# Kernel tuning notes

Hardware: AMD Instinct MI355X
Metric: run time of the kernel (lower is better)

Reference implementation:

```python
import jax, jax.numpy as jnp
import numpy as np

BETA = 8.0  # cfg.memory.beta (inverse temperature)
EPS = 1e-12  # matches F.normalize default eps


def _l2_normalize(x):
    return x / jnp.maximum(jnp.linalg.norm(x, axis=-1, keepdims=True), EPS)


def setup_inputs() -> dict:
    key = jax.random.key(0)
    k1, k2, k3 = jax.random.split(key, 3)
    embeddings = jax.random.normal(k1, (1024, 128), dtype=jnp.float32)   # queries [B, D]
    keys = jax.random.normal(k2, (100000, 128), dtype=jnp.float32)       # stored patterns [N, D]
    labels = jax.random.randint(k3, (100000,), 0, 1000)                  # class per stored pattern [N]
    return {"embeddings": embeddings, "keys": keys, "labels": labels, "n_classes": 1000}


def reference(embeddings, keys, labels, n_classes):
    # store(): keys normalized (normalize_keys=True); values = one_hot(labels)
    k = _l2_normalize(keys)
    # query(): normalize queries, cosine sims, softmax(beta*sims), weighted value sum
    q = _l2_normalize(embeddings)
    sims = q @ k.T                                   # [B, N]
    weights = jax.nn.softmax(BETA * sims, axis=-1)   # [B, N]
    # weights @ one_hot(labels, C) == segment-sum of weights by key label (same math,
    # avoids materializing the dense [N, C] one-hot value matrix)
    out = jax.ops.segment_sum(weights.T, labels, num_segments=n_classes).T  # [B, C]
    return out
```

## Files before the change

### kernel.cpp

```cpp
#include <hip/hip_runtime.h>
#include <math.h>

typedef _Float16 f16;
typedef _Float16 f16x8 __attribute__((ext_vector_type(8)));
typedef float    f32x16 __attribute__((ext_vector_type(16)));
typedef unsigned int uint;
typedef unsigned short u16;

#define B_Q     1024
#define DIM     128
#define N_KEYS  100000
#define NPAD    102400
#define NGP     (NPAD / 32)
#define GPC     8
#define NCHUNK  (NGP / GPC)
#define N_CLS   1000
#define QSCALE  11.541560327111707f
#define CSUM    10
#define NCB     (N_CLS / CSUM)
#define NH      128
#define QGRP    (B_Q / 32)

__global__ void k_hist(const int* __restrict__ labels, uint* __restrict__ hist128) {
    __shared__ uint lh[N_CLS];
    for (int i = threadIdx.x; i < N_CLS; i += blockDim.x) lh[i] = 0;
    __syncthreads();
    const int stride = gridDim.x * blockDim.x;
    for (int i = blockIdx.x * blockDim.x + threadIdx.x; i < N_KEYS; i += stride)
        atomicAdd(&lh[labels[i]], 1u);
    __syncthreads();
    for (int i = threadIdx.x; i < N_CLS; i += blockDim.x)
        hist128[blockIdx.x * N_CLS + i] = lh[i];
}

__global__ void k_scan(const uint* __restrict__ hist128, uint* __restrict__ cursor) {
    __shared__ uint s[1024];
    const int t = threadIdx.x;
    uint v = 0;
    if (t < N_CLS)
        for (int b = 0; b < NH; ++b) v += hist128[b * N_CLS + t];
    s[t] = v; __syncthreads();
    for (int o = 1; o < 1024; o <<= 1) {
        const uint x = (t >= o) ? s[t - o] : 0u;
        __syncthreads();
        s[t] += x;
        __syncthreads();
    }
    if (t < N_CLS) cursor[t] = s[t] - v;
}

__global__ void k_perm(const int* __restrict__ labels, uint* __restrict__ cursor,
                       int* __restrict__ src, u16* __restrict__ kcls) {
    const int n = blockIdx.x * blockDim.x + threadIdx.x;
    if (n >= NPAD) return;
    if (n < N_KEYS) {
        const int lab = labels[n];
        const int pos = (int)atomicAdd(&cursor[lab], 1u);
        src[pos]  = n;
        kcls[pos] = (u16)lab;
    } else {
        src[n]  = -1;
        kcls[n] = (u16)N_CLS;
    }
}

__global__ __launch_bounds__(256)
void k_gather(const float* __restrict__ qm, const float* __restrict__ km,
              const int* __restrict__ src, f16* __restrict__ kf2,
              f16* __restrict__ qf2) {
    __shared__ float ssq[8][32];
    __shared__ float scale[32];
    const int g = blockIdx.x;
    const int t = threadIdx.x;
    const int r = t & 31;
    const int p = t >> 5;
    const bool isq = g >= NGP;

    const float* srow;
    if (isq) srow = qm + (size_t)((g - NGP) * 32 + r) * DIM;
    else {
        const int sr = src[g * 32 + r];
        srow = (sr >= 0) ? km + (size_t)sr * DIM : nullptr;
    }

    float4 v[4];
    float ss = 0.0f;
    if (srow) {
        #pragma unroll
        for (int i = 0; i < 4; ++i) {
            v[i] = *(const float4*)(srow + p * 16 + i * 4);
            ss += v[i].x * v[i].x + v[i].y * v[i].y
                + v[i].z * v[i].z + v[i].w * v[i].w;
        }
    } else {
        #pragma unroll
        for (int i = 0; i < 4; ++i) v[i] = float4{0.f, 0.f, 0.f, 0.f};
    }
    ssq[p][r] = ss;
    __syncthreads();
    if (t < 32) {
        float s = 0.0f;
        #pragma unroll
        for (int i = 0; i < 8; ++i) s += ssq[i][t];
        scale[t] = (isq ? QSCALE : 1.0f) / fmaxf(sqrtf(s), 1e-12f);
    }
    __syncthreads();
    const float sc = scale[r];

    const float f[16] = {v[0].x, v[0].y, v[0].z, v[0].w,
                         v[1].x, v[1].y, v[1].z, v[1].w,
                         v[2].x, v[2].y, v[2].z, v[2].w,
                         v[3].x, v[3].y, v[3].z, v[3].w};
    f16x8 h0, h1;
    #pragma unroll
    for (int j = 0; j < 8; ++j) {
        h0[j] = (f16)(f[j]     * sc);
        h1[j] = (f16)(f[j + 8] * sc);
    }
    f16* dst = isq ? qf2 + (size_t)(g - NGP) * 4096
                   : kf2 + (size_t)g * 4096;
    *(f16x8*)(dst + p * 512 +       r * 8) = h0;
    *(f16x8*)(dst + p * 512 + 256 + r * 8) = h1;
}

__global__ void k_meta(const u16* __restrict__ kcls, int* __restrict__ meta,
                       float* __restrict__ out_t) {
    const int nt = gridDim.x * blockDim.x;
    const float4 z = {0.0f, 0.0f, 0.0f, 0.0f};
    for (int i = blockIdx.x * blockDim.x + threadIdx.x;
         i < N_CLS * B_Q / 4; i += nt)
        ((float4*)out_t)[i] = z;

    const int gid  = blockIdx.x * blockDim.x + threadIdx.x;
    const int g    = gid >> 6;
    const int lane = threadIdx.x & 63;
    if (g >= NGP) return;
    const int  cl = kcls[g * 32 + (lane & 31)];
    const int  ca = __shfl(cl, 0);
    const uint dm = (uint)(__ballot(cl != ca) & 0xffffffffull);
    const int  split = dm ? (__ffs(dm) - 1) : 32;
    const int  cb = (split < 32) ? __shfl(cl, split) : ca;
    if (lane == 0) meta[g] = ca | (cb << 11) | (split << 22);
}

#define FLUSH2(C) {                                                           \
        const float v0 = racc0 + __shfl_xor(racc0, 32);                       \
        const float v1 = racc1 + __shfl_xor(racc1, 32);                       \
        if (lhi == 0) {                                                       \
            atomicAdd(&out_t[(size_t)(C) * B_Q + q00 + l31], v0);             \
            atomicAdd(&out_t[(size_t)(C) * B_Q + q01 + l31], v1);             \
        }                                                                     \
    }

__global__ __launch_bounds__(256, 3)
void class_gemm6(const f16* __restrict__ kf2, const f16* __restrict__ qf2,
                 const int* __restrict__ meta, float* __restrict__ out_t) {
    const int tid  = threadIdx.x;
    const int w    = tid >> 6;
    const int lane = tid & 63;
    const int l31  = lane & 31;
    const int lhi  = lane >> 5;
    const int lhi4 = lhi << 2;

    const int b     = blockIdx.x;
    const int xcd   = b & 7;
    const int s     = b >> 3;
    const int chunk = xcd * (NCHUNK / 8) + (s >> 2);
    const int qquad = s & 3;
    const int g0    = chunk * GPC;

    f16x8 Q0[8], Q1[8];
    {
        const f16* qa = qf2 + (size_t)(qquad * 8 + w * 2) * 4096 + lane * 8;
        #pragma unroll
        for (int kk = 0; kk < 8; ++kk) {
            Q0[kk] = *(const f16x8*)(qa + kk * 512);
            Q1[kk] = *(const f16x8*)(qa + 4096 + kk * 512);
        }
    }
    const int q00 = qquad * 256 + w * 64;
    const int q01 = q00 + 32;

    const int mv = meta[g0 + (lane & (GPC - 1))];

    float racc0 = 0.0f, racc1 = 0.0f;
    int cur = -1;

    for (int i = 0; i < GPC; ++i) {
        const int m     = __shfl(mv, i);
        const int ca    = m & 0x7FF;
        const int cb    = (m >> 11) & 0x7FF;
        const int split = m >> 22;

        const f16* base = kf2 + (size_t)(g0 + i) * 4096 + lane * 8;
        f32x16 c0 = {}, c1 = {};
        #pragma unroll
        for (int kk = 0; kk < 8; ++kk) {
            const f16x8 Kf = *(const f16x8*)(base + kk * 512);
            c0 = __builtin_amdgcn_mfma_f32_32x32x16_f16(Kf, Q0[kk], c0, 0, 0, 0);
            c1 = __builtin_amdgcn_mfma_f32_32x32x16_f16(Kf, Q1[kk], c1, 0, 0, 0);
        }

        if (ca != cur) {
            if (cur >= 0) FLUSH2(cur);
            racc0 = 0.0f; racc1 = 0.0f;
            cur = ca;
        }
        if (split == 32) {
            float ga = 0.0f, gb = 0.0f, gc = 0.0f, gd = 0.0f;
            #pragma unroll
            for (int r = 0; r < 16; r += 2) {
                ga += __builtin_amdgcn_exp2f(c0[r]);
                gb += __builtin_amdgcn_exp2f(c0[r + 1]);
                gc += __builtin_amdgcn_exp2f(c1[r]);
                gd += __builtin_amdgcn_exp2f(c1[r + 1]);
            }
            racc0 += ga + gb;
            racc1 += gc + gd;
        } else {
            float ga = 0.0f, gb = 0.0f, gc = 0.0f, gd = 0.0f;
            float ha = 0.0f, hb = 0.0f, hc = 0.0f, hd = 0.0f;
            #pragma unroll
            for (int r = 0; r < 16; r += 2) {
                const int  kr0 = ((r & 3) + 8 * (r >> 2)) + lhi4;
                const int  kr1 = (((r + 1) & 3) + 8 * ((r + 1) >> 2)) + lhi4;
                const float e0  = __builtin_amdgcn_exp2f(c0[r]);
                const float e0b = __builtin_amdgcn_exp2f(c0[r + 1]);
                const float e1  = __builtin_amdgcn_exp2f(c1[r]);
                const float e1b = __builtin_amdgcn_exp2f(c1[r + 1]);
                const bool inA0 = kr0 < split;
                const bool inA1 = kr1 < split;
                ga += inA0 ? e0  : 0.0f;  ha += inA0 ? 0.0f : e0;
                gb += inA1 ? e0b : 0.0f;  hb += inA1 ? 0.0f : e0b;
                gc += inA0 ? e1  : 0.0f;  hc += inA0 ? 0.0f : e1;
                gd += inA1 ? e1b : 0.0f;  hd += inA1 ? 0.0f : e1b;
            }
            racc0 += ga + gb;
            racc1 += gc + gd;
            FLUSH2(cur);
            racc0 = ha + hb;
            racc1 = hc + hd;
            cur = cb;
        }
    }
    if (cur >= 0) FLUSH2(cur);
}

__global__ __launch_bounds__(1024)
void k_qsum(const float* __restrict__ out_t, float* __restrict__ partial) {
    const int cb = blockIdx.x;
    const int q  = threadIdx.x;
    const float* p = out_t + (size_t)cb * CSUM * B_Q + q;
    float s = 0.0f;
    #pragma unroll
    for (int i = 0; i < CSUM; ++i) s += p[(size_t)i * B_Q];
    partial[cb * B_Q + q] = s;
}

__global__ __launch_bounds__(256)
void k_norm_t(const float* __restrict__ out_t, const float* __restrict__ partial,
              float* __restrict__ out) {
    __shared__ float tile[64 * 65];
    __shared__ float invq[64];
    const int tid  = threadIdx.x;
    const int w    = tid >> 6;
    const int lane = tid & 63;
    const int q0   = blockIdx.x * 64;
    const int c0   = blockIdx.y * 64;

    if (tid < 64) {
        float s = 0.0f;
        for (int cb = 0; cb < NCB; ++cb) s += partial[cb * B_Q + q0 + tid];
        invq[tid] = 1.0f / s;
    }
    #pragma unroll
    for (int i = 0; i < 16; ++i) {
        const int cidx = c0 + w * 16 + i;
        const float v = (cidx < N_CLS) ? out_t[(size_t)cidx * B_Q + q0 + lane] : 0.0f;
        tile[lane * 65 + w * 16 + i] = v;
    }
    __syncthreads();
    #pragma unroll
    for (int j = 0; j < 16; ++j) {
        const int r    = w * 16 + j;
        const int cidx = c0 + lane;
        if (cidx < N_CLS)
            out[(size_t)(q0 + r) * N_CLS + cidx] = tile[r * 65 + lane] * invq[r];
    }
}

extern "C" void kernel_launch(void* const* d_in, const int* in_sizes, int n_in,
                              void* d_out, int out_size, void* d_ws, size_t ws_size,
                              hipStream_t stream) {
    const float* qm     = (const float*)d_in[0];
    const float* km     = (const float*)d_in[1];
    const int*   labels = (const int*)d_in[2];
    float* out = (float*)d_out;

    char* p = (char*)d_ws;
    f16*   kf2     = (f16*)p;   p += (size_t)NPAD * DIM * 2;
    f16*   qf2     = (f16*)p;   p += (size_t)B_Q * DIM * 2;
    float* out_t   = (float*)p; p += (size_t)N_CLS * B_Q * 4;
    float* partial = (float*)p; p += (size_t)NCB * B_Q * 4;
    uint*  cursor  = (uint*)p;  p += N_CLS * 4;
    u16*   kcls    = (u16*)p;   p += (size_t)NPAD * 2;
    int*   meta    = (int*)p;   p += (size_t)NGP * 4;
    int*   src     = (int*)p;   p += (size_t)NPAD * 4;
    uint*  hist128 = (uint*)out_t;

    hipLaunchKernelGGL(k_hist, dim3(NH), dim3(256), 0, stream, labels, hist128);
    hipLaunchKernelGGL(k_scan, dim3(1), dim3(1024), 0, stream, hist128, cursor);
    hipLaunchKernelGGL(k_perm, dim3(NPAD / 256), dim3(256), 0, stream,
                       labels, cursor, src, kcls);
    hipLaunchKernelGGL(k_gather, dim3(NGP + QGRP), dim3(256), 0, stream,
                       qm, km, src, kf2, qf2);
    hipLaunchKernelGGL(k_meta, dim3((NGP * 64 + 255) / 256), dim3(256), 0, stream,
                       kcls, meta, out_t);

    hipLaunchKernelGGL(class_gemm6, dim3(4 * NCHUNK), dim3(256), 0, stream,
                       kf2, qf2, meta, out_t);

    hipLaunchKernelGGL(k_qsum, dim3(NCB), dim3(1024), 0, stream, out_t, partial);
    hipLaunchKernelGGL(k_norm_t, dim3(B_Q / 64, (N_CLS + 63) / 64), dim3(256), 0, stream,
                       out_t, partial, out);
}
```

Baseline: 110.7 us.

## Split GEMM into single-wave blocks, double-buffer K loads, fuse query totals

Replaces the 4-wave GEMM blocks with one-wave blocks and register double-buffers the K fragments, so the next group's loads overlap the current MFMA and exp work. Per-query softmax denominators are now accumulated inside the GEMM through atomics into a qtot buffer, which removes the separate k_qsum pass. The extra zeroing range covers the padding sink row and qtot. This costs more blocks, more atomics and higher register pressure from holding two K buffers.

```diff
diff --git a/kernel.cpp b/kernel.cpp
--- a/kernel.cpp
+++ b/kernel.cpp
@@ -16,8 +16,6 @@
 #define NCHUNK  (NGP / GPC)
 #define N_CLS   1000
 #define QSCALE  11.541560327111707f
-#define CSUM    10
-#define NCB     (N_CLS / CSUM)
 #define NH      128
 #define QGRP    (B_Q / 32)
 
@@ -123,12 +121,12 @@
     *(f16x8*)(dst + p * 512 + 256 + r * 8) = h1;
 }
 
+#define ZFLOATS ((N_CLS + 2) * B_Q)
 __global__ void k_meta(const u16* __restrict__ kcls, int* __restrict__ meta,
                        float* __restrict__ out_t) {
     const int nt = gridDim.x * blockDim.x;
     const float4 z = {0.0f, 0.0f, 0.0f, 0.0f};
-    for (int i = blockIdx.x * blockDim.x + threadIdx.x;
-         i < N_CLS * B_Q / 4; i += nt)
+    for (int i = blockIdx.x * blockDim.x + threadIdx.x; i < ZFLOATS / 4; i += nt)
         ((float4*)out_t)[i] = z;
 
     const int gid  = blockIdx.x * blockDim.x + threadIdx.x;
@@ -146,119 +144,129 @@
 #define FLUSH2(C) {                                                           \
         const float v0 = racc0 + __shfl_xor(racc0, 32);                       \
         const float v1 = racc1 + __shfl_xor(racc1, 32);                       \
+        if ((C) != N_CLS) { tot0 += racc0; tot1 += racc1; }                   \
         if (lhi == 0) {                                                       \
             atomicAdd(&out_t[(size_t)(C) * B_Q + q00 + l31], v0);             \
             atomicAdd(&out_t[(size_t)(C) * B_Q + q01 + l31], v1);             \
         }                                                                     \
     }
 
-__global__ __launch_bounds__(256, 3)
-void class_gemm6(const f16* __restrict__ kf2, const f16* __restrict__ qf2,
-                 const int* __restrict__ meta, float* __restrict__ out_t) {
-    const int tid  = threadIdx.x;
-    const int w    = tid >> 6;
-    const int lane = tid & 63;
+#define LOADK(DST, I) {                                                       \
+        const f16* _kb = kf2 + (size_t)(g0 + (I)) * 4096 + lane * 8;          \
+        _Pragma("unroll")                                                     \
+        for (int kk = 0; kk < 8; ++kk) DST[kk] = *(const f16x8*)(_kb + kk * 512); \
+    }
+
+#define BODY(KB, I) {                                                         \
+        const int m     = __shfl(mv, (I));       \
+        const int ca    = m & 0x7FF;                                          \
+        const int cb    = (m >> 11) & 0x7FF;                                  \
+        const int split = m >> 22;                                            \
+        f32x16 c0 = {}, c1 = {};                                              \
+        _Pragma("unroll")                                                     \
+        for (int kk = 0; kk < 8; ++kk) {                                      \
+            c0 = __builtin_amdgcn_mfma_f32_32x32x16_f16(KB[kk], Q0[kk], c0, 0, 0, 0); \
+            c1 = __builtin_amdgcn_mfma_f32_32x32x16_f16(KB[kk], Q1[kk], c1, 0, 0, 0); \
+        }                                                                     \
+        if (ca != cur) {                                                      \
+            if (cur >= 0) FLUSH2(cur);                                        \
+            racc0 = 0.0f; racc1 = 0.0f;                                       \
+            cur = ca;                                                         \
+        }                                                                     \
+        if (split == 32) {                                                    \
+            float ga = 0.f, gb = 0.f, gc = 0.f, gd = 0.f;                     \
+            _Pragma("unroll")                                                 \
+            for (int r = 0; r < 16; r += 2) {                                 \
+                ga += __builtin_amdgcn_exp2f(c0[r]);                          \
+                gb += __builtin_amdgcn_exp2f(c0[r + 1]);                      \
+                gc += __builtin_amdgcn_exp2f(c1[r]);                          \
+                gd += __builtin_amdgcn_exp2f(c1[r + 1]);                      \
+            }                                                                 \
+            racc0 += ga + gb;                                                 \
+            racc1 += gc + gd;                                                 \
+        } else {                                                              \
+            float ga = 0.f, gb = 0.f, gc = 0.f, gd = 0.f;                     \
+            float ha = 0.f, hb = 0.f, hc = 0.f, hd = 0.f;                     \
+            _Pragma("unroll")                                                 \
+            for (int r = 0; r < 16; r += 2) {                                 \
+                const int  kr0 = ((r & 3) + 8 * (r >> 2)) + lhi4;             \
+                const int  kr1 = (((r + 1) & 3) + 8 * ((r + 1) >> 2)) + lhi4; \
+                const float e0  = __builtin_amdgcn_exp2f(c0[r]);              \
+                const float e0b = __builtin_amdgcn_exp2f(c0[r + 1]);          \
+                const float e1  = __builtin_amdgcn_exp2f(c1[r]);              \
+                const float e1b = __builtin_amdgcn_exp2f(c1[r + 1]);          \
+                const bool inA0 = kr0 < split;                                \
+                const bool inA1 = kr1 < split;                                \
+                ga += inA0 ? e0  : 0.0f;  ha += inA0 ? 0.0f : e0;             \
+                gb += inA1 ? e0b : 0.0f;  hb += inA1 ? 0.0f : e0b;            \
+                gc += inA0 ? e1  : 0.0f;  hc += inA0 ? 0.0f : e1;             \
+                gd += inA1 ? e1b : 0.0f;  hd += inA1 ? 0.0f : e1b;            \
+            }                                                                 \
+            racc0 += ga + gb;                                                 \
+            racc1 += gc + gd;                                                 \
+            FLUSH2(cur);                                                      \
+            racc0 = ha + hb;                                                  \
+            racc1 = hc + hd;                                                  \
+            cur = cb;                                                         \
+        }                                                                     \
+    }
+
+__global__ __launch_bounds__(64)
+void class_gemm7(const f16* __restrict__ kf2, const f16* __restrict__ qf2,
+                 const int* __restrict__ meta, float* __restrict__ out_t,
+                 float* __restrict__ qtot) {
+    const int lane = threadIdx.x & 63;
     const int l31  = lane & 31;
     const int lhi  = lane >> 5;
     const int lhi4 = lhi << 2;
 
     const int b     = blockIdx.x;
     const int xcd   = b & 7;
-    const int s     = b >> 3;
-    const int chunk = xcd * (NCHUNK / 8) + (s >> 2);
-    const int qquad = s & 3;
+    const int u     = b >> 3;
+    const int chunk = xcd * (NCHUNK / 8) + (u >> 4);
+    const int qquad = (u >> 2) & 3;
+    const int wsub  = u & 3;
     const int g0    = chunk * GPC;
 
     f16x8 Q0[8], Q1[8];
     {
-        const f16* qa = qf2 + (size_t)(qquad * 8 + w * 2) * 4096 + lane * 8;
+        const f16* qa = qf2 + (size_t)(qquad * 8 + wsub * 2) * 4096 + lane * 8;
         #pragma unroll
         for (int kk = 0; kk < 8; ++kk) {
             Q0[kk] = *(const f16x8*)(qa + kk * 512);
             Q1[kk] = *(const f16x8*)(qa + 4096 + kk * 512);
         }
     }
-    const int q00 = qquad * 256 + w * 64;
+    const int q00 = qquad * 256 + wsub * 64;
     const int q01 = q00 + 32;
 
     const int mv = meta[g0 + (lane & (GPC - 1))];
 
     float racc0 = 0.0f, racc1 = 0.0f;
+    float tot0  = 0.0f, tot1  = 0.0f;
     int cur = -1;
 
-    for (int i = 0; i < GPC; ++i) {
-        const int m     = __shfl(mv, i);
-        const int ca    = m & 0x7FF;
-        const int cb    = (m >> 11) & 0x7FF;
-        const int split = m >> 22;
-
-        const f16* base = kf2 + (size_t)(g0 + i) * 4096 + lane * 8;
-        f32x16 c0 = {}, c1 = {};
-        #pragma unroll
-        for (int kk = 0; kk < 8; ++kk) {
-            const f16x8 Kf = *(const f16x8*)(base + kk * 512);
-            c0 = __builtin_amdgcn_mfma_f32_32x32x16_f16(Kf, Q0[kk], c0, 0, 0, 0);
-            c1 = __builtin_amdgcn_mfma_f32_32x32x16_f16(Kf, Q1[kk], c1, 0, 0, 0);
+    f16x8 K0[8], K1[8];
+    LOADK(K0, 0);
+    #pragma unroll
+    for (int ii = 0; ii < GPC / 2; ++ii) {
+        { const int i = 2 * ii;     if (i + 1 < GPC) LOADK(K1, i + 1); BODY(K0, i); }
+        { const int i = 2 * ii + 1; if (i + 1 < GPC) LOADK(K0, i + 1); BODY(K1, i); }
+    }
+    if (cur >= 0) FLUSH2(cur);
+
+    {
+        const float t0 = tot0 + __shfl_xor(tot0, 32);
+        const float t1 = tot1 + __shfl_xor(tot1, 32);
+        if (lhi == 0) {
+            atomicAdd(&qtot[q00 + l31], t0);
+            atomicAdd(&qtot[q01 + l31], t1);
         }
-
-        if (ca != cur) {
-            if (cur >= 0) FLUSH2(cur);
-            racc0 = 0.0f; racc1 = 0.0f;
-            cur = ca;
-        }
-        if (split == 32) {
-            float ga = 0.0f, gb = 0.0f, gc = 0.0f, gd = 0.0f;
-            #pragma unroll
-            for (int r = 0; r < 16; r += 2) {
-                ga += __builtin_amdgcn_exp2f(c0[r]);
-                gb += __builtin_amdgcn_exp2f(c0[r + 1]);
-                gc += __builtin_amdgcn_exp2f(c1[r]);
-                gd += __builtin_amdgcn_exp2f(c1[r + 1]);
-            }
-            racc0 += ga + gb;
-            racc1 += gc + gd;
-        } else {
-            float ga = 0.0f, gb = 0.0f, gc = 0.0f, gd = 0.0f;
-            float ha = 0.0f, hb = 0.0f, hc = 0.0f, hd = 0.0f;
-            #pragma unroll
-            for (int r = 0; r < 16; r += 2) {
-                const int  kr0 = ((r & 3) + 8 * (r >> 2)) + lhi4;
-                const int  kr1 = (((r + 1) & 3) + 8 * ((r + 1) >> 2)) + lhi4;
-                const float e0  = __builtin_amdgcn_exp2f(c0[r]);
-                const float e0b = __builtin_amdgcn_exp2f(c0[r + 1]);
-                const float e1  = __builtin_amdgcn_exp2f(c1[r]);
-                const float e1b = __builtin_amdgcn_exp2f(c1[r + 1]);
-                const bool inA0 = kr0 < split;
-                const bool inA1 = kr1 < split;
-                ga += inA0 ? e0  : 0.0f;  ha += inA0 ? 0.0f : e0;
-                gb += inA1 ? e0b : 0.0f;  hb += inA1 ? 0.0f : e0b;
-                gc += inA0 ? e1  : 0.0f;  hc += inA0 ? 0.0f : e1;
-                gd += inA1 ? e1b : 0.0f;  hd += inA1 ? 0.0f : e1b;
-            }
-            racc0 += ga + gb;
-            racc1 += gc + gd;
-            FLUSH2(cur);
-            racc0 = ha + hb;
-            racc1 = hc + hd;
-            cur = cb;
-        }
-    }
-    if (cur >= 0) FLUSH2(cur);
-}
-
-__global__ __launch_bounds__(1024)
-void k_qsum(const float* __restrict__ out_t, float* __restrict__ partial) {
-    const int cb = blockIdx.x;
-    const int q  = threadIdx.x;
-    const float* p = out_t + (size_t)cb * CSUM * B_Q + q;
-    float s = 0.0f;
-    #pragma unroll
-    for (int i = 0; i < CSUM; ++i) s += p[(size_t)i * B_Q];
-    partial[cb * B_Q + q] = s;
+    }
 }
 
 __global__ __launch_bounds__(256)
-void k_norm_t(const float* __restrict__ out_t, const float* __restrict__ partial,
+void k_norm_t(const float* __restrict__ out_t, const float* __restrict__ qtot,
               float* __restrict__ out) {
     __shared__ float tile[64 * 65];
     __shared__ float invq[64];
@@ -268,11 +276,8 @@
     const int q0   = blockIdx.x * 64;
     const int c0   = blockIdx.y * 64;
 
-    if (tid < 64) {
-        float s = 0.0f;
-        for (int cb = 0; cb < NCB; ++cb) s += partial[cb * B_Q + q0 + tid];
-        invq[tid] = 1.0f / s;
-    }
+    if (tid < 64) invq[tid] = 1.0f / qtot[q0 + tid];
+
     #pragma unroll
     for (int i = 0; i < 16; ++i) {
         const int cidx = c0 + w * 16 + i;
@@ -301,11 +306,13 @@
     f16*   kf2     = (f16*)p;   p += (size_t)NPAD * DIM * 2;
     f16*   qf2     = (f16*)p;   p += (size_t)B_Q * DIM * 2;
     float* out_t   = (float*)p; p += (size_t)N_CLS * B_Q * 4;
-    float* partial = (float*)p; p += (size_t)NCB * B_Q * 4;
+    float* sink    = (float*)p; p += (size_t)B_Q * 4;
+    float* qtot    = (float*)p; p += (size_t)B_Q * 4;
     uint*  cursor  = (uint*)p;  p += N_CLS * 4;
     u16*   kcls    = (u16*)p;   p += (size_t)NPAD * 2;
     int*   meta    = (int*)p;   p += (size_t)NGP * 4;
     int*   src     = (int*)p;   p += (size_t)NPAD * 4;
+    (void)sink;
     uint*  hist128 = (uint*)out_t;
 
     hipLaunchKernelGGL(k_hist, dim3(NH), dim3(256), 0, stream, labels, hist128);
@@ -317,10 +324,9 @@
     hipLaunchKernelGGL(k_meta, dim3((NGP * 64 + 255) / 256), dim3(256), 0, stream,
                        kcls, meta, out_t);
 
-    hipLaunchKernelGGL(class_gemm6, dim3(4 * NCHUNK), dim3(256), 0, stream,
-                       kf2, qf2, meta, out_t);
-
-    hipLaunchKernelGGL(k_qsum, dim3(NCB), dim3(1024), 0, stream, out_t, partial);
+    hipLaunchKernelGGL(class_gemm7, dim3(16 * NCHUNK), dim3(64), 0, stream,
+                       kf2, qf2, meta, out_t, qtot);
+
     hipLaunchKernelGGL(k_norm_t, dim3(B_Q / 64, (N_CLS + 63) / 64), dim3(256), 0, stream,
-                       out_t, partial, out);
-}
+                       out_t, qtot, out);
+}
```

Measured after the change: 101.6 us. 1.09x faster.
